# Optimization experiments

Measured on AMD Instinct MI355X. Metric: run time of the kernel, lower is better.

The kernel has to match this reference:

```python
import jax, jax.numpy as jnp
import numpy as np

N = 50000   # nodes
E = 1600000 # edges
G = 512     # graphs in batch
IN_DIM, EMBED, H, D = 64, 128, 4, 32
D1, D2, D3 = 128, 64, 16
NEG_SLOPE = 0.2  # DGL GATConv default


def setup_inputs() -> dict:
    key = jax.random.key(0)
    ks = jax.random.split(key, 16)
    def glorot(k, shape):
        fan = shape[0] + shape[-1]
        return jax.random.normal(k, shape, jnp.float32) * jnp.sqrt(2.0 / fan)
    return {
        "feature": jax.random.normal(ks[0], (N, IN_DIM), jnp.float32),
        "src": jax.random.randint(ks[1], (E,), 0, N, jnp.int32),
        "dst": jax.random.randint(ks[2], (E,), 0, N, jnp.int32),
        "graph_ids": jnp.sort(jax.random.randint(ks[3], (N,), 0, G, jnp.int32)),
        "W0": glorot(ks[4], (IN_DIM, EMBED)), "b0": jnp.zeros((EMBED,), jnp.float32),
        "Wfc": glorot(ks[5], (EMBED, H * D)),
        "attn_l": glorot(ks[6], (H, D)), "attn_r": glorot(ks[7], (H, D)),
        "gat_bias": jnp.zeros((H * D,), jnp.float32),
        "W1": glorot(ks[8], (H * D, D1)), "b1": jnp.zeros((D1,), jnp.float32),
        "W2": glorot(ks[9], (D1, D2)), "b2": jnp.zeros((D2,), jnp.float32),
        "W3": glorot(ks[10], (D2, D3)), "b3": jnp.zeros((D3,), jnp.float32),
    }


def reference(feature, src, dst, graph_ids, W0, b0, Wfc, attn_l, attn_r,
              gat_bias, W1, b1, W2, b2, W3, b3):
    # initial dense embed
    h = feature @ W0 + b0                                   # [N, EMBED]
    # GATConv
    feat = (h @ Wfc).reshape(N, H, D)                       # [N,H,D]
    el = jnp.einsum('nhd,hd->nh', feat, attn_l)             # [N,H]
    er = jnp.einsum('nhd,hd->nh', feat, attn_r)
    e = jax.nn.leaky_relu(el[src] + er[dst], NEG_SLOPE)     # [E,H]
    # segment softmax over incoming edges of each dst node
    m = jax.ops.segment_max(e, dst, num_segments=N)         # [N,H]
    ex = jnp.exp(e - m[dst])                                # [E,H]
    denom = jax.ops.segment_sum(ex, dst, num_segments=N)    # [N,H]
    a = ex / denom[dst]                                     # [E,H]
    msg = a[:, :, None] * feat[src]                         # [E,H,D]
    rst = jax.ops.segment_sum(msg, dst, num_segments=N)     # [N,H,D]
    rst = rst + gat_bias.reshape(1, H, D)
    hn = rst.reshape(N, H * D)
    # AvgPooling per graph
    sums = jax.ops.segment_sum(hn, graph_ids, num_segments=G)           # [G,H*D]
    cnts = jax.ops.segment_sum(jnp.ones((N,), hn.dtype), graph_ids, num_segments=G)
    hg = sums / jnp.maximum(cnts, 1.0)[:, None]
    # dense head
    out = jax.nn.elu(hg)
    out = jax.nn.elu(out @ W1 + b1)
    out = jax.nn.elu(out @ W2 + b2)
    out = out @ W3 + b3                                     # [G, D3]
    atten = a[:, :, None]                                   # [E,H,1] like DGL
    return out, atten
```

## Files before the change

kernel.cpp:

```cpp
#include <hip/hip_runtime.h>
#include <hip/hip_fp16.h>
#include <math.h>

#define N_NODES 50000
#define E_EDGES 1600000
#define G_GRAPHS 512
#define IN_DIM 64
#define EMBED 128
#define HD 128
#define NHEAD 4
#define D1 128
#define D2 64
#define D3 16
#define NEG_SLOPE 0.2f
#define NB ((N_NODES + 127) >> 7)
#define PT_TILE 4096
#define PT_BLOCKS ((E_EDGES + PT_TILE - 1) / PT_TILE)
#define FB_CAP 8192

typedef float vfloat4 __attribute__((ext_vector_type(4)));
typedef float vfloat2 __attribute__((ext_vector_type(2)));
typedef unsigned short ushort_t;

static __device__ __forceinline__ float leaky(float x) { return x > 0.f ? x : NEG_SLOPE * x; }

__global__ void __launch_bounds__(256) k0hg(const int* __restrict__ dst, int* __restrict__ ghist,
                                            const float* __restrict__ W0, const float* __restrict__ b0,
                                            const float* __restrict__ Wfc, float* __restrict__ Wc,
                                            float* __restrict__ bc) {
    __shared__ int lh[NB];
    const int t = threadIdx.x;
    if (blockIdx.x < PT_BLOCKS) {
        for (int i = t; i < NB; i += 256) lh[i] = 0;
        __syncthreads();
        const long e0 = (long)blockIdx.x * PT_TILE;
#pragma unroll
        for (int k = 0; k < PT_TILE / 256; ++k) {
            long e = e0 + t + k * 256;
            if (e < E_EDGES) atomicAdd(&lh[dst[e] >> 7], 1);
        }
        __syncthreads();
        for (int i = t; i < NB; i += 256) {
            int v = lh[i];
            if (v) atomicAdd(&ghist[i], v);
        }
    } else {
        int tid = (int)(blockIdx.x - PT_BLOCKS) * 256 + t;
        if (tid < IN_DIM * HD) {
            int i = tid >> 7, j = tid & 127;
            float acc = 0.f;
            for (int k = 0; k < EMBED; ++k) acc += W0[i * EMBED + k] * Wfc[k * HD + j];
            Wc[tid] = acc;
        } else if (tid < IN_DIM * HD + HD) {
            int j = tid - IN_DIM * HD;
            float acc = 0.f;
            for (int k = 0; k < EMBED; ++k) acc += b0[k] * Wfc[k * HD + j];
            bc[j] = acc;
        }
    }
}

__global__ void __launch_bounds__(256) k1_gemm(const float* __restrict__ A,
                                               const float* __restrict__ W,
                                               const float* __restrict__ b,
                                               const float* __restrict__ attn_l,
                                               const float* __restrict__ attn_r,
                                               unsigned char* __restrict__ feat,
                                               float* __restrict__ el,
                                               float* __restrict__ er) {
    __shared__ __align__(16) float Ws[IN_DIM * HD];
    __shared__ __align__(16) float As[64][68];
    const int t = threadIdx.x;
    const int cc = t & 31;
    const int rt = t >> 5;
    const int c0 = cc * 4;
    const int r0 = rt * 8;
    const int row0 = blockIdx.x * 64;

    {
        const float4* Wg = (const float4*)W;
        float4* Wl = (float4*)Ws;
#pragma unroll
        for (int j = 0; j < (IN_DIM * HD / 4) / 256; ++j) Wl[t + j * 256] = Wg[t + j * 256];
    }
#pragma unroll
    for (int j = 0; j < 4; ++j) {
        int i2 = t + j * 256;
        int row = i2 >> 4, kq = i2 & 15;
        int gr = row0 + row;
        float4 v = (gr < N_NODES) ? *(const float4*)(A + (size_t)gr * IN_DIM + kq * 4)
                                  : make_float4(0.f, 0.f, 0.f, 0.f);
        *(float4*)&As[row][kq * 4] = v;
    }
    __syncthreads();

    float acc[8][4];
#pragma unroll
    for (int i = 0; i < 8; ++i)
#pragma unroll
        for (int j = 0; j < 4; ++j) acc[i][j] = 0.f;

    for (int k4 = 0; k4 < IN_DIM / 4; ++k4) {
        vfloat4 w0 = *(const vfloat4*)&Ws[(k4 * 4 + 0) * HD + c0];
        vfloat4 w1 = *(const vfloat4*)&Ws[(k4 * 4 + 1) * HD + c0];
        vfloat4 w2 = *(const vfloat4*)&Ws[(k4 * 4 + 2) * HD + c0];
        vfloat4 w3 = *(const vfloat4*)&Ws[(k4 * 4 + 3) * HD + c0];
#pragma unroll
        for (int i = 0; i < 8; ++i) {
            vfloat4 a = *(const vfloat4*)&As[r0 + i][k4 * 4];
#pragma unroll
            for (int j = 0; j < 4; ++j)
                acc[i][j] += a.x * w0[j] + a.y * w1[j] + a.z * w2[j] + a.w * w3[j];
        }
    }

    {
        vfloat4 bcv = *(const vfloat4*)(b + c0);
#pragma unroll
        for (int i = 0; i < 8; ++i)
#pragma unroll
            for (int j = 0; j < 4; ++j) acc[i][j] += bcv[j];
    }

#pragma unroll
    for (int i = 0; i < 8; ++i) {
        int gr = row0 + r0 + i;
        if (gr < N_NODES) {
            unsigned int ww = __builtin_amdgcn_cvt_pk_fp8_f32(acc[i][0], acc[i][1], 0, false);
            ww = __builtin_amdgcn_cvt_pk_fp8_f32(acc[i][2], acc[i][3], ww, true);
            *(unsigned int*)(feat + (size_t)gr * HD + c0) = ww;
        }
    }

    {
        vfloat4 al = *(const vfloat4*)(attn_l + c0);
        vfloat4 ar = *(const vfloat4*)(attn_r + c0);
        float pl[8], pr[8];
#pragma unroll
        for (int i = 0; i < 8; ++i) {
            pl[i] = acc[i][0] * al[0] + acc[i][1] * al[1] + acc[i][2] * al[2] + acc[i][3] * al[3];
            pr[i] = acc[i][0] * ar[0] + acc[i][1] * ar[1] + acc[i][2] * ar[2] + acc[i][3] * ar[3];
        }
#pragma unroll
        for (int off = 1; off <= 4; off <<= 1) {
#pragma unroll
            for (int i = 0; i < 8; ++i) {
                pl[i] += __shfl_xor(pl[i], off);
                pr[i] += __shfl_xor(pr[i], off);
            }
        }
        if ((cc & 7) == 0) {
            const int h = cc >> 3;
#pragma unroll
            for (int i = 0; i < 8; ++i) {
                int gr = row0 + r0 + i;
                if (gr < N_NODES) {
                    el[gr * 4 + h] = pl[i];
                    er[gr * 4 + h] = pr[i];
                }
            }
        }
    }
}

__global__ void __launch_bounds__(64) sc_scan(const int* __restrict__ ghist,
                                              int* __restrict__ coarse_start,
                                              int* __restrict__ cursorp) {
    const int lane = threadIdx.x;
    int run = 0;
    for (int c = 0; c < (NB + 63) / 64; ++c) {
        int i = c * 64 + lane;
        int v = (i < NB) ? ghist[i] : 0;
        int incl = v;
#pragma unroll
        for (int off = 1; off < 64; off <<= 1) {
            int o = __shfl_up(incl, off, 64);
            if (lane >= off) incl += o;
        }
        if (i < NB) {
            coarse_start[i] = run + incl - v;
            cursorp[i] = run + incl - v;
        }
        run += __shfl(incl, 63, 64);
    }
    if (lane == 0) coarse_start[NB] = E_EDGES;
}

__global__ void __launch_bounds__(256) pt_partition(const int* __restrict__ src,
                                                    const int* __restrict__ dst,
                                                    int* __restrict__ cursorp,
                                                    unsigned int* __restrict__ part) {
    __shared__ int hist[4][NB];
    __shared__ int tot[NB], offs[NB], base_s[NB];
    __shared__ int lcur[4][NB];
    __shared__ unsigned int stage[PT_TILE];
    const int t = threadIdx.x, lane = t & 63, wid = t >> 6;
    const long e0 = (long)blockIdx.x * PT_TILE;
    const int cnt = (int)min((long)PT_TILE, (long)E_EDGES - e0);
    for (int i = t; i < NB; i += 256) {
        hist[0][i] = 0; hist[1][i] = 0; hist[2][i] = 0; hist[3][i] = 0;
    }
    __syncthreads();
    unsigned int v[PT_TILE / 256];
#pragma unroll
    for (int k = 0; k < PT_TILE / 256; ++k) {
        int i = t + k * 256;
        if (i < cnt) {
            int d = dst[e0 + i];
            v[k] = ((unsigned int)d << 16) | (unsigned int)src[e0 + i];
            atomicAdd(&hist[wid][d >> 7], 1);
        } else v[k] = 0xFFFFFFFFu;
    }
    __syncthreads();
    for (int i = t; i < NB; i += 256) {
        int h0 = hist[0][i], h1 = hist[1][i], h2 = hist[2][i], h3 = hist[3][i];
        hist[0][i] = 0; hist[1][i] = h0; hist[2][i] = h0 + h1; hist[3][i] = h0 + h1 + h2;
        tot[i] = h0 + h1 + h2 + h3;
    }
    __syncthreads();
    if (wid == 0) {
        int run = 0;
        for (int c = 0; c < (NB + 63) / 64; ++c) {
            int i = c * 64 + lane;
            int vv = (i < NB) ? tot[i] : 0;
            int incl = vv;
#pragma unroll
            for (int off = 1; off < 64; off <<= 1) {
                int o = __shfl_up(incl, off, 64);
                if (lane >= off) incl += o;
            }
            if (i < NB) offs[i] = run + incl - vv;
            run += __shfl(incl, 63, 64);
        }
    }
    __syncthreads();
    for (int i = t; i < NB; i += 256) {
        int tt = tot[i];
        base_s[i] = tt ? atomicAdd(&cursorp[i], tt) : 0;
        int ob = offs[i];
        lcur[0][i] = ob + hist[0][i];
        lcur[1][i] = ob + hist[1][i];
        lcur[2][i] = ob + hist[2][i];
        lcur[3][i] = ob + hist[3][i];
    }
    __syncthreads();
#pragma unroll
    for (int k = 0; k < PT_TILE / 256; ++k) {
        if (v[k] != 0xFFFFFFFFu) {
            int b = v[k] >> 23;
            int pos = atomicAdd(&lcur[wid][b], 1);
            stage[pos] = v[k];
        }
    }
    __syncthreads();
    for (int i = t; i < cnt; i += 256) {
        unsigned int p = stage[i];
        int b = p >> 23;
        part[base_s[b] + (i - offs[b])] = p & 0x7FFFFFu;
    }
}

__global__ void __launch_bounds__(256) fb_fill(const unsigned int* __restrict__ part,
                                               const int* __restrict__ coarse_start,
                                               int* __restrict__ rowstart,
                                               ushort_t* __restrict__ csr_src) {
    const int b = blockIdx.x, t = threadIdx.x, lane = t & 63, wid = t >> 6;
    const int s0 = coarse_start[b], s1 = coarse_start[b + 1];
    const int cnt = s1 - s0;
    __shared__ int degl[4][128], totl[128], offl[128], curl[4][128];
    __shared__ ushort_t lsrc[FB_CAP];
    if (t < 128) { degl[0][t] = 0; degl[1][t] = 0; degl[2][t] = 0; degl[3][t] = 0; }
    __syncthreads();
    for (int i = t; i < cnt; i += 256) {
        unsigned int p = part[s0 + i];
        atomicAdd(&degl[wid][p >> 16], 1);
    }
    __syncthreads();
    if (t < 128) {
        int d0 = degl[0][t], d1 = degl[1][t], d2 = degl[2][t], d3 = degl[3][t];
        degl[0][t] = 0; degl[1][t] = d0; degl[2][t] = d0 + d1; degl[3][t] = d0 + d1 + d2;
        totl[t] = d0 + d1 + d2 + d3;
    }
    __syncthreads();
    if (wid == 0) {
        int run = 0;
        for (int c = 0; c < 2; ++c) {
            int i = c * 64 + lane;
            int vv = totl[i];
            int incl = vv;
#pragma unroll
            for (int off = 1; off < 64; off <<= 1) {
                int o = __shfl_up(incl, off, 64);
                if (lane >= off) incl += o;
            }
            offl[i] = run + incl - vv;
            run += __shfl(incl, 63, 64);
        }
    }
    __syncthreads();
    if (t < 128) {
        int ob = offl[t];
        curl[0][t] = ob + degl[0][t];
        curl[1][t] = ob + degl[1][t];
        curl[2][t] = ob + degl[2][t];
        curl[3][t] = ob + degl[3][t];
        int node = (b << 7) + t;
        if (node < N_NODES) rowstart[node] = s0 + ob;
    }
    if (b == 0 && t == 0) rowstart[N_NODES] = E_EDGES;
    __syncthreads();
    if (cnt <= FB_CAP) {
        for (int i = t; i < cnt; i += 256) {
            unsigned int p = part[s0 + i];
            int pos = atomicAdd(&curl[wid][p >> 16], 1);
            lsrc[pos] = (ushort_t)(p & 0xFFFFu);
        }
        __syncthreads();
        for (int i = t; i < cnt; i += 256) csr_src[s0 + i] = lsrc[i];
    } else {
        for (int i = t; i < cnt; i += 256) {
            unsigned int p = part[s0 + i];
            int pos = atomicAdd(&curl[wid][p >> 16], 1);
            csr_src[s0 + pos] = (ushort_t)(p & 0xFFFFu);
        }
    }
}

__global__ void __launch_bounds__(256) k6_aggregate(
    const ushort_t* __restrict__ csr_src, const int* __restrict__ rowstart,
    const float* __restrict__ el, const float* __restrict__ er,
    const unsigned char* __restrict__ feat, const float* __restrict__ gat_bias,
    float* __restrict__ er_rd, float* __restrict__ hn) {
    __shared__ uint2 s_pk[4][64][4];
    const int wid = threadIdx.x >> 6;
    const int lane = threadIdx.x & 63;
    const int n = blockIdx.x * 4 + wid;
    if (n >= N_NODES) return;
    const int start = rowstart[n];
    const int end = rowstart[n + 1];
    const int deg = end - start;

    const int e0 = lane >> 2;
    const int h = lane & 3;
    const float erh = er[n * 4 + h];
    float sm = 0.f;
    for (int base = 0; base < deg; base += 16) {
        const int e = base + e0;
        const bool v = e < deg;
        if (v) {
            const int s = csr_src[start + e];
            const float ex = __expf(leaky(el[s * 4 + h] + erh));
            sm += ex;
            if (e < 64)
                s_pk[wid][e][h] = make_uint2((unsigned int)s << 7, __float_as_uint(ex));
        }
    }
#pragma unroll
    for (int off = 4; off <= 32; off <<= 1) sm += __shfl_xor(sm, off);
    const float rd = sm > 0.f ? 1.f / sm : 0.f;
    if (lane < 4) {
        er_rd[(size_t)n * 8 + lane] = erh;
        er_rd[(size_t)n * 8 + 4 + lane] = rd;
    }

    const int g4 = lane >> 4, gl = lane & 15;
    const int h2 = gl >> 2;
    const float rdh = __shfl(rd, h2);
    vfloat2 acc0 = {0.f, 0.f}, acc1 = {0.f, 0.f}, acc2 = {0.f, 0.f}, acc3 = {0.f, 0.f};

    if (deg <= 64) {
        const uint2* pk = &s_pk[wid][0][h2];
        const unsigned char* fg = feat + (gl << 3);
        int idx = g4;
        for (; idx + 4 < deg; idx += 8) {
            const uint2 pA = pk[idx * 4];
            const uint2 pB = pk[(idx + 4) * 4];
            const uint2 wA = *(const uint2*)(fg + pA.x);
            const uint2 wB = *(const uint2*)(fg + pB.x);
            const float exA = __uint_as_float(pA.y);
            const float exB = __uint_as_float(pB.y);
            const vfloat2 eA = {exA, exA}, eB = {exB, exB};
            acc0 += eA * __builtin_amdgcn_cvt_pk_f32_fp8(wA.x, false);
            acc1 += eA * __builtin_amdgcn_cvt_pk_f32_fp8(wA.x, true);
            acc2 += eA * __builtin_amdgcn_cvt_pk_f32_fp8(wA.y, false);
            acc3 += eA * __builtin_amdgcn_cvt_pk_f32_fp8(wA.y, true);
            acc0 += eB * __builtin_amdgcn_cvt_pk_f32_fp8(wB.x, false);
            acc1 += eB * __builtin_amdgcn_cvt_pk_f32_fp8(wB.x, true);
            acc2 += eB * __builtin_amdgcn_cvt_pk_f32_fp8(wB.y, false);
            acc3 += eB * __builtin_amdgcn_cvt_pk_f32_fp8(wB.y, true);
        }
        if (idx < deg) {
            const uint2 p = pk[idx * 4];
            const uint2 w = *(const uint2*)(fg + p.x);
            const float ex = __uint_as_float(p.y);
            const vfloat2 ev = {ex, ex};
            acc0 += ev * __builtin_amdgcn_cvt_pk_f32_fp8(w.x, false);
            acc1 += ev * __builtin_amdgcn_cvt_pk_f32_fp8(w.x, true);
            acc2 += ev * __builtin_amdgcn_cvt_pk_f32_fp8(w.y, false);
            acc3 += ev * __builtin_amdgcn_cvt_pk_f32_fp8(w.y, true);
        }
    } else {
        const float erh2 = __shfl(erh, h2);
        const unsigned char* fg = feat + (gl << 3);
        for (int e = start + g4; e < end; e += 4) {
            const unsigned int s = csr_src[e];
            const float ex = __expf(leaky(el[s * 4 + h2] + erh2));
            const vfloat2 ev = {ex, ex};
            const uint2 w = *(const uint2*)(fg + ((size_t)s << 7));
            acc0 += ev * __builtin_amdgcn_cvt_pk_f32_fp8(w.x, false);
            acc1 += ev * __builtin_amdgcn_cvt_pk_f32_fp8(w.x, true);
            acc2 += ev * __builtin_amdgcn_cvt_pk_f32_fp8(w.y, false);
            acc3 += ev * __builtin_amdgcn_cvt_pk_f32_fp8(w.y, true);
        }
    }
    {
        const vfloat2 rv = {rdh, rdh};
        acc0 *= rv; acc1 *= rv; acc2 *= rv; acc3 *= rv;
    }
#pragma unroll
    for (int off = 16; off <= 32; off <<= 1) {
        acc0.x += __shfl_xor(acc0.x, off);
        acc0.y += __shfl_xor(acc0.y, off);
        acc1.x += __shfl_xor(acc1.x, off);
        acc1.y += __shfl_xor(acc1.y, off);
        acc2.x += __shfl_xor(acc2.x, off);
        acc2.y += __shfl_xor(acc2.y, off);
        acc3.x += __shfl_xor(acc3.x, off);
        acc3.y += __shfl_xor(acc3.y, off);
    }
    if (lane < 16) {
        const float4 b0 = ((const float4*)gat_bias)[gl * 2];
        const float4 b1 = ((const float4*)gat_bias)[gl * 2 + 1];
        float4* hp = (float4*)(hn + (size_t)n * HD + gl * 8);
        hp[0] = make_float4(acc0.x + b0.x, acc0.y + b0.y, acc1.x + b0.z, acc1.y + b0.w);
        hp[1] = make_float4(acc2.x + b1.x, acc2.y + b1.y, acc3.x + b1.z, acc3.y + b1.w);
    }
}

__global__ void __launch_bounds__(256) k6b_attn(
    const int* __restrict__ src, const int* __restrict__ dst,
    const float* __restrict__ el, const float* __restrict__ er_rd,
    float* __restrict__ a_out) {
    int e = blockIdx.x * 256 + threadIdx.x;
    if (e >= E_EDGES) return;
    const int s = src[e], d = dst[e];
    const float4 el4 = *(const float4*)(el + s * 4);
    const float4 er4 = *(const float4*)(er_rd + (size_t)d * 8);
    const float4 r4 = *(const float4*)(er_rd + (size_t)d * 8 + 4);
    vfloat4 a;
    a.x = __expf(leaky(el4.x + er4.x)) * r4.x;
    a.y = __expf(leaky(el4.y + er4.y)) * r4.y;
    a.z = __expf(leaky(el4.z + er4.z)) * r4.z;
    a.w = __expf(leaky(el4.w + er4.w)) * r4.w;
    __builtin_nontemporal_store(a, (vfloat4*)a_out + e);
}

__global__ void __launch_bounds__(512) k7_pool_mlp(
    const float* __restrict__ hn, const int* __restrict__ graph_ids,
    const float* __restrict__ W1, const float* __restrict__ b1,
    const float* __restrict__ W2, const float* __restrict__ b2,
    const float* __restrict__ W3, const float* __restrict__ b3,
    float* __restrict__ out) {
    const int g = blockIdx.x, t = threadIdx.x;
    const int tt = t & 127, part = t >> 7;
    __shared__ int bounds[2];
    __shared__ double pool[4][128];
    __shared__ double x[128], y[128];
    if (t < 2) {
        const int target = g + t;
        int lo = 0, hi = N_NODES;
        while (lo < hi) {
            int mid = (lo + hi) >> 1;
            if (graph_ids[mid] < target) lo = mid + 1; else hi = mid;
        }
        bounds[t] = lo;
    }
    __syncthreads();
    const int lo = bounds[0], hi = bounds[1];
    double s = 0.0;
    for (int n = lo + part; n < hi; n += 4) s += (double)hn[(size_t)n * HD + tt];
    pool[part][tt] = s;
    __syncthreads();
    if (t < 128) {
        const double cnt = (double)(hi - lo);
        const double sum = pool[0][t] + pool[1][t] + pool[2][t] + pool[3][t];
        const double v = sum / fmax(cnt, 1.0);
        x[t] = v > 0.0 ? v : expm1(v);
    }
    __syncthreads();
    if (t < 128) {
        double acc = (double)b1[t];
        for (int k = 0; k < HD; ++k) acc += x[k] * (double)W1[k * D1 + t];
        y[t] = acc > 0.0 ? acc : expm1(acc);
    }
    __syncthreads();
    if (t < D2) {
        double a2 = (double)b2[t];
        for (int k = 0; k < D1; ++k) a2 += y[k] * (double)W2[k * D2 + t];
        x[t] = a2 > 0.0 ? a2 : expm1(a2);
    }
    __syncthreads();
    if (t < D3) {
        double a3 = (double)b3[t];
        for (int k = 0; k < D2; ++k) a3 += x[k] * (double)W3[k * D3 + t];
        out[g * D3 + t] = (float)a3;
    }
}

extern "C" void kernel_launch(void* const* d_in, const int* in_sizes, int n_in,
                              void* d_out, int out_size, void* d_ws, size_t ws_size,
                              hipStream_t stream) {
    const float* feature = (const float*)d_in[0];
    const int* src = (const int*)d_in[1];
    const int* dst = (const int*)d_in[2];
    const int* graph_ids = (const int*)d_in[3];
    const float* W0 = (const float*)d_in[4];
    const float* b0 = (const float*)d_in[5];
    const float* Wfc = (const float*)d_in[6];
    const float* attn_l = (const float*)d_in[7];
    const float* attn_r = (const float*)d_in[8];
    const float* gat_bias = (const float*)d_in[9];
    const float* W1 = (const float*)d_in[10];
    const float* b1 = (const float*)d_in[11];
    const float* W2 = (const float*)d_in[12];
    const float* b2 = (const float*)d_in[13];
    const float* W3 = (const float*)d_in[14];
    const float* b3 = (const float*)d_in[15];

    char* ws = (char*)d_ws;
    size_t off = 0;
    auto carve = [&](size_t bytes) -> void* {
        void* p = ws + off;
        off += (bytes + 255) & ~(size_t)255;
        return p;
    };
    int* ghist = (int*)carve((size_t)NB * 4);
    const size_t zero_span = off;
    int* coarse_start = (int*)carve((size_t)(NB + 1) * 4);
    int* cursorp = (int*)carve((size_t)NB * 4);
    float* Wc = (float*)carve((size_t)IN_DIM * HD * 4);
    float* bc = (float*)carve((size_t)HD * 4);
    unsigned char* feat = (unsigned char*)carve((size_t)N_NODES * HD);
    float* el = (float*)carve((size_t)N_NODES * 4 * 4);
    float* er = (float*)carve((size_t)N_NODES * 4 * 4);
    float* er_rd = (float*)carve((size_t)N_NODES * 8 * 4);
    int* rowstart = (int*)carve((size_t)(N_NODES + 1) * 4);
    unsigned int* part = (unsigned int*)carve((size_t)E_EDGES * 4);
    ushort_t* csr_src = (ushort_t*)carve((size_t)E_EDGES * 2);

    float* out = (float*)d_out;
    float* hn = out + G_GRAPHS * D3;
    float* a_out = hn;

    (void)hipMemsetAsync(d_ws, 0, zero_span, stream);
    k0hg<<<PT_BLOCKS + 33, 256, 0, stream>>>(dst, ghist, W0, b0, Wfc, Wc, bc);
    k1_gemm<<<(N_NODES + 63) / 64, 256, 0, stream>>>(feature, Wc, bc, attn_l, attn_r,
                                                     feat, el, er);
    sc_scan<<<1, 64, 0, stream>>>(ghist, coarse_start, cursorp);
    pt_partition<<<PT_BLOCKS, 256, 0, stream>>>(src, dst, cursorp, part);
    fb_fill<<<NB, 256, 0, stream>>>(part, coarse_start, rowstart, csr_src);
    k6_aggregate<<<(N_NODES + 3) / 4, 256, 0, stream>>>(csr_src, rowstart, el, er, feat,
                                                        gat_bias, er_rd, hn);
    k7_pool_mlp<<<G_GRAPHS, 512, 0, stream>>>(hn, graph_ids, W1, b1, W2, b2, W3, b3, out);
    k6b_attn<<<(E_EDGES + 255) / 256, 256, 0, stream>>>(src, dst, el, er_rd, a_out);
}
```

Measured before the change: 250.4 us.

## Use nontemporal loads/stores, double partition tile, merge fb_fill coarse bins per block

Measured after the change: 283.1 us. 1.13x slower.

```diff
diff --git a/kernel.cpp b/kernel.cpp
--- a/kernel.cpp
+++ b/kernel.cpp
@@ -14,7 +14,7 @@
 #define D3 16
 #define NEG_SLOPE 0.2f
 #define NB ((N_NODES + 127) >> 7)
-#define PT_TILE 4096
+#define PT_TILE 8192
 #define PT_BLOCKS ((E_EDGES + PT_TILE - 1) / PT_TILE)
 #define FB_CAP 8192
 
@@ -37,7 +37,7 @@
 #pragma unroll
         for (int k = 0; k < PT_TILE / 256; ++k) {
             long e = e0 + t + k * 256;
-            if (e < E_EDGES) atomicAdd(&lh[dst[e] >> 7], 1);
+            if (e < E_EDGES) atomicAdd(&lh[__builtin_nontemporal_load(&dst[e]) >> 7], 1);
         }
         __syncthreads();
         for (int i = t; i < NB; i += 256) {
@@ -88,9 +88,10 @@
         int i2 = t + j * 256;
         int row = i2 >> 4, kq = i2 & 15;
         int gr = row0 + row;
-        float4 v = (gr < N_NODES) ? *(const float4*)(A + (size_t)gr * IN_DIM + kq * 4)
-                                  : make_float4(0.f, 0.f, 0.f, 0.f);
-        *(float4*)&As[row][kq * 4] = v;
+        vfloat4 v = {0.f, 0.f, 0.f, 0.f};
+        if (gr < N_NODES)
+            v = __builtin_nontemporal_load((const vfloat4*)(A + (size_t)gr * IN_DIM + kq * 4));
+        *(vfloat4*)&As[row][kq * 4] = v;
     }
     __syncthreads();
 
@@ -206,8 +207,9 @@
     for (int k = 0; k < PT_TILE / 256; ++k) {
         int i = t + k * 256;
         if (i < cnt) {
-            int d = dst[e0 + i];
-            v[k] = ((unsigned int)d << 16) | (unsigned int)src[e0 + i];
+            int d = __builtin_nontemporal_load(&dst[e0 + i]);
+            int s = __builtin_nontemporal_load(&src[e0 + i]);
+            v[k] = ((unsigned int)d << 16) | (unsigned int)s;
             atomicAdd(&hist[wid][d >> 7], 1);
         } else v[k] = 0xFFFFFFFFu;
     }
@@ -256,7 +258,7 @@
     for (int i = t; i < cnt; i += 256) {
         unsigned int p = stage[i];
         int b = p >> 23;
-        part[base_s[b] + (i - offs[b])] = p & 0x7FFFFFu;
+        __builtin_nontemporal_store(p & 0x7FFFFFu, &part[base_s[b] + (i - offs[b])]);
     }
 }
 
@@ -264,65 +266,71 @@
                                                const int* __restrict__ coarse_start,
                                                int* __restrict__ rowstart,
                                                ushort_t* __restrict__ csr_src) {
-    const int b = blockIdx.x, t = threadIdx.x, lane = t & 63, wid = t >> 6;
-    const int s0 = coarse_start[b], s1 = coarse_start[b + 1];
-    const int cnt = s1 - s0;
+    const int t = threadIdx.x, lane = t & 63, wid = t >> 6;
     __shared__ int degl[4][128], totl[128], offl[128], curl[4][128];
     __shared__ ushort_t lsrc[FB_CAP];
-    if (t < 128) { degl[0][t] = 0; degl[1][t] = 0; degl[2][t] = 0; degl[3][t] = 0; }
-    __syncthreads();
-    for (int i = t; i < cnt; i += 256) {
-        unsigned int p = part[s0 + i];
-        atomicAdd(&degl[wid][p >> 16], 1);
-    }
-    __syncthreads();
-    if (t < 128) {
-        int d0 = degl[0][t], d1 = degl[1][t], d2 = degl[2][t], d3 = degl[3][t];
-        degl[0][t] = 0; degl[1][t] = d0; degl[2][t] = d0 + d1; degl[3][t] = d0 + d1 + d2;
-        totl[t] = d0 + d1 + d2 + d3;
-    }
-    __syncthreads();
-    if (wid == 0) {
-        int run = 0;
-        for (int c = 0; c < 2; ++c) {
-            int i = c * 64 + lane;
-            int vv = totl[i];
-            int incl = vv;
-#pragma unroll
-            for (int off = 1; off < 64; off <<= 1) {
-                int o = __shfl_up(incl, off, 64);
-                if (lane >= off) incl += o;
-            }
-            offl[i] = run + incl - vv;
-            run += __shfl(incl, 63, 64);
-        }
-    }
-    __syncthreads();
-    if (t < 128) {
-        int ob = offl[t];
-        curl[0][t] = ob + degl[0][t];
-        curl[1][t] = ob + degl[1][t];
-        curl[2][t] = ob + degl[2][t];
-        curl[3][t] = ob + degl[3][t];
-        int node = (b << 7) + t;
-        if (node < N_NODES) rowstart[node] = s0 + ob;
-    }
-    if (b == 0 && t == 0) rowstart[N_NODES] = E_EDGES;
-    __syncthreads();
-    if (cnt <= FB_CAP) {
+    if (blockIdx.x == 0 && t == 0) rowstart[N_NODES] = E_EDGES;
+    for (int sub = 0; sub < 2; ++sub) {
+        const int b = (int)blockIdx.x * 2 + sub;
+        if (b >= NB) break;
+        const int s0 = coarse_start[b], s1 = coarse_start[b + 1];
+        const int cnt = s1 - s0;
+        if (t < 128) { degl[0][t] = 0; degl[1][t] = 0; degl[2][t] = 0; degl[3][t] = 0; }
+        __syncthreads();
         for (int i = t; i < cnt; i += 256) {
             unsigned int p = part[s0 + i];
-            int pos = atomicAdd(&curl[wid][p >> 16], 1);
-            lsrc[pos] = (ushort_t)(p & 0xFFFFu);
-        }
-        __syncthreads();
-        for (int i = t; i < cnt; i += 256) csr_src[s0 + i] = lsrc[i];
-    } else {
-        for (int i = t; i < cnt; i += 256) {
-            unsigned int p = part[s0 + i];
-            int pos = atomicAdd(&curl[wid][p >> 16], 1);
-            csr_src[s0 + pos] = (ushort_t)(p & 0xFFFFu);
-        }
+            atomicAdd(&degl[wid][p >> 16], 1);
+        }
+        __syncthreads();
+        if (t < 128) {
+            int d0 = degl[0][t], d1 = degl[1][t], d2 = degl[2][t], d3 = degl[3][t];
+            degl[0][t] = 0; degl[1][t] = d0; degl[2][t] = d0 + d1; degl[3][t] = d0 + d1 + d2;
+            totl[t] = d0 + d1 + d2 + d3;
+        }
+        __syncthreads();
+        if (wid == 0) {
+            int run = 0;
+            for (int c = 0; c < 2; ++c) {
+                int i = c * 64 + lane;
+                int vv = totl[i];
+                int incl = vv;
+#pragma unroll
+                for (int off = 1; off < 64; off <<= 1) {
+                    int o = __shfl_up(incl, off, 64);
+                    if (lane >= off) incl += o;
+                }
+                offl[i] = run + incl - vv;
+                run += __shfl(incl, 63, 64);
+            }
+        }
+        __syncthreads();
+        if (t < 128) {
+            int ob = offl[t];
+            curl[0][t] = ob + degl[0][t];
+            curl[1][t] = ob + degl[1][t];
+            curl[2][t] = ob + degl[2][t];
+            curl[3][t] = ob + degl[3][t];
+            int node = (b << 7) + t;
+            if (node < N_NODES) rowstart[node] = s0 + ob;
+        }
+        __syncthreads();
+        if (cnt <= FB_CAP) {
+            for (int i = t; i < cnt; i += 256) {
+                unsigned int p = part[s0 + i];
+                int pos = atomicAdd(&curl[wid][p >> 16], 1);
+                lsrc[pos] = (ushort_t)(p & 0xFFFFu);
+            }
+            __syncthreads();
+            for (int i = t; i < cnt; i += 256)
+                __builtin_nontemporal_store(lsrc[i], &csr_src[s0 + i]);
+        } else {
+            for (int i = t; i < cnt; i += 256) {
+                unsigned int p = part[s0 + i];
+                int pos = atomicAdd(&curl[wid][p >> 16], 1);
+                csr_src[s0 + pos] = (ushort_t)(p & 0xFFFFu);
+            }
+        }
+        __syncthreads();
     }
 }
 
@@ -348,7 +356,7 @@
         const int e = base + e0;
         const bool v = e < deg;
         if (v) {
-            const int s = csr_src[start + e];
+            const int s = __builtin_nontemporal_load(&csr_src[start + e]);
             const float ex = __expf(leaky(el[s * 4 + h] + erh));
             sm += ex;
             if (e < 64)
@@ -359,8 +367,8 @@
     for (int off = 4; off <= 32; off <<= 1) sm += __shfl_xor(sm, off);
     const float rd = sm > 0.f ? 1.f / sm : 0.f;
     if (lane < 4) {
-        er_rd[(size_t)n * 8 + lane] = erh;
-        er_rd[(size_t)n * 8 + 4 + lane] = rd;
+        __builtin_nontemporal_store(erh, &er_rd[(size_t)n * 8 + lane]);
+        __builtin_nontemporal_store(rd, &er_rd[(size_t)n * 8 + 4 + lane]);
     }
 
     const int g4 = lane >> 4, gl = lane & 15;
@@ -403,7 +411,7 @@
         const float erh2 = __shfl(erh, h2);
         const unsigned char* fg = feat + (gl << 3);
         for (int e = start + g4; e < end; e += 4) {
-            const unsigned int s = csr_src[e];
+            const unsigned int s = __builtin_nontemporal_load(&csr_src[e]);
             const float ex = __expf(leaky(el[s * 4 + h2] + erh2));
             const vfloat2 ev = {ex, ex};
             const uint2 w = *(const uint2*)(fg + ((size_t)s << 7));
@@ -431,9 +439,11 @@
     if (lane < 16) {
         const float4 b0 = ((const float4*)gat_bias)[gl * 2];
         const float4 b1 = ((const float4*)gat_bias)[gl * 2 + 1];
-        float4* hp = (float4*)(hn + (size_t)n * HD + gl * 8);
-        hp[0] = make_float4(acc0.x + b0.x, acc0.y + b0.y, acc1.x + b0.z, acc1.y + b0.w);
-        hp[1] = make_float4(acc2.x + b1.x, acc2.y + b1.y, acc3.x + b1.z, acc3.y + b1.w);
+        vfloat4 o0 = {acc0.x + b0.x, acc0.y + b0.y, acc1.x + b0.z, acc1.y + b0.w};
+        vfloat4 o1 = {acc2.x + b1.x, acc2.y + b1.y, acc3.x + b1.z, acc3.y + b1.w};
+        vfloat4* hp = (vfloat4*)(hn + (size_t)n * HD + gl * 8);
+        __builtin_nontemporal_store(o0, hp);
+        __builtin_nontemporal_store(o1, hp + 1);
     }
 }
 
@@ -443,7 +453,8 @@
     float* __restrict__ a_out) {
     int e = blockIdx.x * 256 + threadIdx.x;
     if (e >= E_EDGES) return;
-    const int s = src[e], d = dst[e];
+    const int s = __builtin_nontemporal_load(&src[e]);
+    const int d = __builtin_nontemporal_load(&dst[e]);
     const float4 el4 = *(const float4*)(el + s * 4);
     const float4 er4 = *(const float4*)(er_rd + (size_t)d * 8);
     const float4 r4 = *(const float4*)(er_rd + (size_t)d * 8 + 4);
@@ -478,7 +489,8 @@
     __syncthreads();
     const int lo = bounds[0], hi = bounds[1];
     double s = 0.0;
-    for (int n = lo + part; n < hi; n += 4) s += (double)hn[(size_t)n * HD + tt];
+    for (int n = lo + part; n < hi; n += 4)
+        s += (double)__builtin_nontemporal_load(&hn[(size_t)n * HD + tt]);
     pool[part][tt] = s;
     __syncthreads();
     if (t < 128) {
@@ -558,7 +570,7 @@
                                                      feat, el, er);
     sc_scan<<<1, 64, 0, stream>>>(ghist, coarse_start, cursorp);
     pt_partition<<<PT_BLOCKS, 256, 0, stream>>>(src, dst, cursorp, part);
-    fb_fill<<<NB, 256, 0, stream>>>(part, coarse_start, rowstart, csr_src);
+    fb_fill<<<(NB + 1) / 2, 256, 0, stream>>>(part, coarse_start, rowstart, csr_src);
     k6_aggregate<<<(N_NODES + 3) / 4, 256, 0, stream>>>(csr_src, rowstart, el, er, feat,
                                                         gat_bias, er_rd, hn);
     k7_pool_mlp<<<G_GRAPHS, 512, 0, stream>>>(hn, graph_ids, W1, b1, W2, b2, W3, b3, out);
```

## Fuse per-graph pooling into aggregation via atomics and retune partition kernels

Applied to the files above, without the earlier changes.

New measurement: 441.5 us. +76.3%, slower.

```diff
diff --git a/kernel.cpp b/kernel.cpp
--- a/kernel.cpp
+++ b/kernel.cpp
@@ -14,7 +14,7 @@
 #define D3 16
 #define NEG_SLOPE 0.2f
 #define NB ((N_NODES + 127) >> 7)
-#define PT_TILE 4096
+#define PT_TILE 8192
 #define PT_BLOCKS ((E_EDGES + PT_TILE - 1) / PT_TILE)
 #define FB_CAP 8192
 
@@ -88,9 +88,10 @@
         int i2 = t + j * 256;
         int row = i2 >> 4, kq = i2 & 15;
         int gr = row0 + row;
-        float4 v = (gr < N_NODES) ? *(const float4*)(A + (size_t)gr * IN_DIM + kq * 4)
-                                  : make_float4(0.f, 0.f, 0.f, 0.f);
-        *(float4*)&As[row][kq * 4] = v;
+        vfloat4 v = {0.f, 0.f, 0.f, 0.f};
+        if (gr < N_NODES)
+            v = __builtin_nontemporal_load((const vfloat4*)(A + (size_t)gr * IN_DIM + kq * 4));
+        *(vfloat4*)&As[row][kq * 4] = v;
     }
     __syncthreads();
 
@@ -264,65 +265,70 @@
                                                const int* __restrict__ coarse_start,
                                                int* __restrict__ rowstart,
                                                ushort_t* __restrict__ csr_src) {
-    const int b = blockIdx.x, t = threadIdx.x, lane = t & 63, wid = t >> 6;
-    const int s0 = coarse_start[b], s1 = coarse_start[b + 1];
-    const int cnt = s1 - s0;
+    const int t = threadIdx.x, lane = t & 63, wid = t >> 6;
     __shared__ int degl[4][128], totl[128], offl[128], curl[4][128];
     __shared__ ushort_t lsrc[FB_CAP];
-    if (t < 128) { degl[0][t] = 0; degl[1][t] = 0; degl[2][t] = 0; degl[3][t] = 0; }
-    __syncthreads();
-    for (int i = t; i < cnt; i += 256) {
-        unsigned int p = part[s0 + i];
-        atomicAdd(&degl[wid][p >> 16], 1);
-    }
-    __syncthreads();
-    if (t < 128) {
-        int d0 = degl[0][t], d1 = degl[1][t], d2 = degl[2][t], d3 = degl[3][t];
-        degl[0][t] = 0; degl[1][t] = d0; degl[2][t] = d0 + d1; degl[3][t] = d0 + d1 + d2;
-        totl[t] = d0 + d1 + d2 + d3;
-    }
-    __syncthreads();
-    if (wid == 0) {
-        int run = 0;
-        for (int c = 0; c < 2; ++c) {
-            int i = c * 64 + lane;
-            int vv = totl[i];
-            int incl = vv;
-#pragma unroll
-            for (int off = 1; off < 64; off <<= 1) {
-                int o = __shfl_up(incl, off, 64);
-                if (lane >= off) incl += o;
-            }
-            offl[i] = run + incl - vv;
-            run += __shfl(incl, 63, 64);
-        }
-    }
-    __syncthreads();
-    if (t < 128) {
-        int ob = offl[t];
-        curl[0][t] = ob + degl[0][t];
-        curl[1][t] = ob + degl[1][t];
-        curl[2][t] = ob + degl[2][t];
-        curl[3][t] = ob + degl[3][t];
-        int node = (b << 7) + t;
-        if (node < N_NODES) rowstart[node] = s0 + ob;
-    }
-    if (b == 0 && t == 0) rowstart[N_NODES] = E_EDGES;
-    __syncthreads();
-    if (cnt <= FB_CAP) {
+    if (blockIdx.x == 0 && t == 0) rowstart[N_NODES] = E_EDGES;
+    for (int sub = 0; sub < 2; ++sub) {
+        const int b = (int)blockIdx.x * 2 + sub;
+        if (b >= NB) break;
+        const int s0 = coarse_start[b], s1 = coarse_start[b + 1];
+        const int cnt = s1 - s0;
+        if (t < 128) { degl[0][t] = 0; degl[1][t] = 0; degl[2][t] = 0; degl[3][t] = 0; }
+        __syncthreads();
         for (int i = t; i < cnt; i += 256) {
             unsigned int p = part[s0 + i];
-            int pos = atomicAdd(&curl[wid][p >> 16], 1);
-            lsrc[pos] = (ushort_t)(p & 0xFFFFu);
-        }
-        __syncthreads();
-        for (int i = t; i < cnt; i += 256) csr_src[s0 + i] = lsrc[i];
-    } else {
-        for (int i = t; i < cnt; i += 256) {
-            unsigned int p = part[s0 + i];
-            int pos = atomicAdd(&curl[wid][p >> 16], 1);
-            csr_src[s0 + pos] = (ushort_t)(p & 0xFFFFu);
-        }
+            atomicAdd(&degl[wid][p >> 16], 1);
+        }
+        __syncthreads();
+        if (t < 128) {
+            int d0 = degl[0][t], d1 = degl[1][t], d2 = degl[2][t], d3 = degl[3][t];
+            degl[0][t] = 0; degl[1][t] = d0; degl[2][t] = d0 + d1; degl[3][t] = d0 + d1 + d2;
+            totl[t] = d0 + d1 + d2 + d3;
+        }
+        __syncthreads();
+        if (wid == 0) {
+            int run = 0;
+            for (int c = 0; c < 2; ++c) {
+                int i = c * 64 + lane;
+                int vv = totl[i];
+                int incl = vv;
+#pragma unroll
+                for (int off = 1; off < 64; off <<= 1) {
+                    int o = __shfl_up(incl, off, 64);
+                    if (lane >= off) incl += o;
+                }
+                offl[i] = run + incl - vv;
+                run += __shfl(incl, 63, 64);
+            }
+        }
+        __syncthreads();
+        if (t < 128) {
+            int ob = offl[t];
+            curl[0][t] = ob + degl[0][t];
+            curl[1][t] = ob + degl[1][t];
+            curl[2][t] = ob + degl[2][t];
+            curl[3][t] = ob + degl[3][t];
+            int node = (b << 7) + t;
+            if (node < N_NODES) rowstart[node] = s0 + ob;
+        }
+        __syncthreads();
+        if (cnt <= FB_CAP) {
+            for (int i = t; i < cnt; i += 256) {
+                unsigned int p = part[s0 + i];
+                int pos = atomicAdd(&curl[wid][p >> 16], 1);
+                lsrc[pos] = (ushort_t)(p & 0xFFFFu);
+            }
+            __syncthreads();
+            for (int i = t; i < cnt; i += 256) csr_src[s0 + i] = lsrc[i];
+        } else {
+            for (int i = t; i < cnt; i += 256) {
+                unsigned int p = part[s0 + i];
+                int pos = atomicAdd(&curl[wid][p >> 16], 1);
+                csr_src[s0 + pos] = (ushort_t)(p & 0xFFFFu);
+            }
+        }
+        __syncthreads();
     }
 }
 
@@ -330,7 +336,8 @@
     const ushort_t* __restrict__ csr_src, const int* __restrict__ rowstart,
     const float* __restrict__ el, const float* __restrict__ er,
     const unsigned char* __restrict__ feat, const float* __restrict__ gat_bias,
-    float* __restrict__ er_rd, float* __restrict__ hn) {
+    const int* __restrict__ graph_ids,
+    float* __restrict__ er_rd, float* __restrict__ pool) {
     __shared__ uint2 s_pk[4][64][4];
     const int wid = threadIdx.x >> 6;
     const int lane = threadIdx.x & 63;
@@ -431,9 +438,16 @@
     if (lane < 16) {
         const float4 b0 = ((const float4*)gat_bias)[gl * 2];
         const float4 b1 = ((const float4*)gat_bias)[gl * 2 + 1];
-        float4* hp = (float4*)(hn + (size_t)n * HD + gl * 8);
-        hp[0] = make_float4(acc0.x + b0.x, acc0.y + b0.y, acc1.x + b0.z, acc1.y + b0.w);
-        hp[1] = make_float4(acc2.x + b1.x, acc2.y + b1.y, acc3.x + b1.z, acc3.y + b1.w);
+        const int gid = graph_ids[n];
+        float* pp = pool + (size_t)gid * HD + gl * 8;
+        atomicAdd(pp + 0, acc0.x + b0.x);
+        atomicAdd(pp + 1, acc0.y + b0.y);
+        atomicAdd(pp + 2, acc1.x + b0.z);
+        atomicAdd(pp + 3, acc1.y + b0.w);
+        atomicAdd(pp + 4, acc2.x + b1.x);
+        atomicAdd(pp + 5, acc2.y + b1.y);
+        atomicAdd(pp + 6, acc3.x + b1.z);
+        atomicAdd(pp + 7, acc3.y + b1.w);
     }
 }
 
@@ -455,16 +469,14 @@
     __builtin_nontemporal_store(a, (vfloat4*)a_out + e);
 }
 
-__global__ void __launch_bounds__(512) k7_pool_mlp(
-    const float* __restrict__ hn, const int* __restrict__ graph_ids,
+__global__ void __launch_bounds__(128) k7_mlp(
+    const float* __restrict__ pool, const int* __restrict__ graph_ids,
     const float* __restrict__ W1, const float* __restrict__ b1,
     const float* __restrict__ W2, const float* __restrict__ b2,
     const float* __restrict__ W3, const float* __restrict__ b3,
     float* __restrict__ out) {
     const int g = blockIdx.x, t = threadIdx.x;
-    const int tt = t & 127, part = t >> 7;
     __shared__ int bounds[2];
-    __shared__ double pool[4][128];
     __shared__ double x[128], y[128];
     if (t < 2) {
         const int target = g + t;
@@ -476,19 +488,13 @@
         bounds[t] = lo;
     }
     __syncthreads();
-    const int lo = bounds[0], hi = bounds[1];
-    double s = 0.0;
-    for (int n = lo + part; n < hi; n += 4) s += (double)hn[(size_t)n * HD + tt];
-    pool[part][tt] = s;
-    __syncthreads();
-    if (t < 128) {
-        const double cnt = (double)(hi - lo);
-        const double sum = pool[0][t] + pool[1][t] + pool[2][t] + pool[3][t];
-        const double v = sum / fmax(cnt, 1.0);
+    const double cnt = (double)(bounds[1] - bounds[0]);
+    {
+        const double v = (double)pool[(size_t)g * HD + t] / fmax(cnt, 1.0);
         x[t] = v > 0.0 ? v : expm1(v);
     }
     __syncthreads();
-    if (t < 128) {
+    {
         double acc = (double)b1[t];
         for (int k = 0; k < HD; ++k) acc += x[k] * (double)W1[k * D1 + t];
         y[t] = acc > 0.0 ? acc : expm1(acc);
@@ -535,6 +541,7 @@
         return p;
     };
     int* ghist = (int*)carve((size_t)NB * 4);
+    float* pool = (float*)carve((size_t)G_GRAPHS * HD * 4);
     const size_t zero_span = off;
     int* coarse_start = (int*)carve((size_t)(NB + 1) * 4);
     int* cursorp = (int*)carve((size_t)NB * 4);
@@ -549,8 +556,7 @@
     ushort_t* csr_src = (ushort_t*)carve((size_t)E_EDGES * 2);
 
     float* out = (float*)d_out;
-    float* hn = out + G_GRAPHS * D3;
-    float* a_out = hn;
+    float* a_out = out + G_GRAPHS * D3;
 
     (void)hipMemsetAsync(d_ws, 0, zero_span, stream);
     k0hg<<<PT_BLOCKS + 33, 256, 0, stream>>>(dst, ghist, W0, b0, Wfc, Wc, bc);
@@ -558,9 +564,9 @@
                                                      feat, el, er);
     sc_scan<<<1, 64, 0, stream>>>(ghist, coarse_start, cursorp);
     pt_partition<<<PT_BLOCKS, 256, 0, stream>>>(src, dst, cursorp, part);
-    fb_fill<<<NB, 256, 0, stream>>>(part, coarse_start, rowstart, csr_src);
+    fb_fill<<<(NB + 1) / 2, 256, 0, stream>>>(part, coarse_start, rowstart, csr_src);
     k6_aggregate<<<(N_NODES + 3) / 4, 256, 0, stream>>>(csr_src, rowstart, el, er, feat,
-                                                        gat_bias, er_rd, hn);
-    k7_pool_mlp<<<G_GRAPHS, 512, 0, stream>>>(hn, graph_ids, W1, b1, W2, b2, W3, b3, out);
+                                                        gat_bias, graph_ids, er_rd, pool);
+    k7_mlp<<<G_GRAPHS, 128, 0, stream>>>(pool, graph_ids, W1, b1, W2, b2, W3, b3, out);
     k6b_attn<<<(E_EDGES + 255) / 256, 256, 0, stream>>>(src, dst, el, er_rd, a_out);
 }
```
